# Optimization experiments

Measured on AMD Instinct MI355X. Metric: run time of the kernel, lower is better.

## Reference

```python
import jax, jax.numpy as jnp
import numpy as np

N, C, H, K, HID = 131072, 256, 8, 128, 1024
SCALE = (C // H) ** -0.5  # 1/sqrt(32)


def layernorm(x, g, b, eps=1e-5):
    mu = jnp.mean(x, axis=-1, keepdims=True)
    var = jnp.var(x, axis=-1, keepdims=True)
    return (x - mu) * jax.lax.rsqrt(var + eps) * g + b


def setup_inputs() -> dict:
    key = jax.random.key(0)
    ks = jax.random.split(key, 8)
    feat = jax.random.normal(ks[0], (N, C), dtype=jnp.float32)
    order = jax.random.permutation(ks[1], N)  # serialized order (gather)
    inverse = jnp.argsort(order)              # scatter back (unpad identity)
    s = 0.02
    return {
        "feat": feat,
        "ln1_g": jnp.ones((C,), jnp.float32), "ln1_b": jnp.zeros((C,), jnp.float32),
        "w_qkv": jax.random.normal(ks[2], (C, 3 * C), jnp.float32) * s,
        "b_qkv": jnp.zeros((3 * C,), jnp.float32),
        "w_proj": jax.random.normal(ks[3], (C, C), jnp.float32) * s,
        "b_proj": jnp.zeros((C,), jnp.float32),
        "ln2_g": jnp.ones((C,), jnp.float32), "ln2_b": jnp.zeros((C,), jnp.float32),
        "w1": jax.random.normal(ks[4], (C, HID), jnp.float32) * s,
        "b1": jnp.zeros((HID,), jnp.float32),
        "w2": jax.random.normal(ks[5], (HID, C), jnp.float32) * s,
        "b2": jnp.zeros((C,), jnp.float32),
        "order": order,
        "inverse": inverse,
    }


def attention(x, w_qkv, b_qkv, w_proj, b_proj, order, inverse):
    D = C // H
    qkv = x @ w_qkv + b_qkv                       # [N, 3C]
    qkv = qkv[order]                              # gather to serialized order
    qkv = qkv.reshape(-1, K, 3, H, D)             # [P, K, 3, H, D]
    q, k, v = jnp.moveaxis(qkv, 2, 0)             # each [P, K, H, D]
    q = jnp.swapaxes(q, 1, 2)                     # [P, H, K, D]
    k = jnp.swapaxes(k, 1, 2)
    v = jnp.swapaxes(v, 1, 2)
    attn = jnp.einsum("phkd,phjd->phkj", q * SCALE, k)  # [P, H, K, K]
    attn = jax.nn.softmax(attn, axis=-1)
    out = jnp.einsum("phkj,phjd->phkd", attn, v)  # [P, H, K, D]
    out = jnp.swapaxes(out, 1, 2).reshape(-1, C)  # [N, C]
    out = out[inverse]                            # scatter back to input order
    return out @ w_proj + b_proj


def reference(feat, ln1_g, ln1_b, w_qkv, b_qkv, w_proj, b_proj,
              ln2_g, ln2_b, w1, b1, w2, b2, order, inverse):
    # pre-norm transformer block: x + attn(ln1(x)); x + mlp(ln2(x))
    x = feat
    x = x + attention(layernorm(x, ln1_g, ln1_b), w_qkv, b_qkv, w_proj, b_proj, order, inverse)
    h = layernorm(x, ln2_g, ln2_b)
    h = jax.nn.gelu(h @ w1 + b1) @ w2 + b2
    return x + h
```

## Files before the change

### kernel.cpp

```cpp
#include <hip/hip_runtime.h>
#include <hip/hip_bf16.h>

typedef __hip_bfloat16 bf16;
typedef __bf16 bf16x8 __attribute__((ext_vector_type(8)));
typedef float f32x4 __attribute__((ext_vector_type(4)));

#define N_TOK 131072
#define C_DIM 256
#define HID_DIM 1024

__device__ __forceinline__ void async_copy16(void* lds, const void* g) {
  __builtin_amdgcn_global_load_lds(
      (const __attribute__((address_space(1))) void*)g,
      (__attribute__((address_space(3))) void*)lds, 16, 0, 0);
}

__device__ __forceinline__ float fast_rcp(float x) {
#if __has_builtin(__builtin_amdgcn_rcpf)
  return __builtin_amdgcn_rcpf(x);
#else
  return 1.f / x;
#endif
}

__device__ __forceinline__ float fast_gelu(float x) {
  float y = 0.7978845608028654f * x * (1.f + 0.044715f * x * x);
  float e = __expf(2.f * y);
  float th = 1.f - 2.f * fast_rcp(e + 1.f);
  return 0.5f * x * (1.f + th);
}

__global__ void ln_bf16_kernel(const float* __restrict__ x,
                               const float* __restrict__ g,
                               const float* __restrict__ b,
                               bf16* __restrict__ out) {
  int row = blockIdx.x * 4 + threadIdx.y;
  int lane = threadIdx.x;
  size_t base = (size_t)row * C_DIM + lane * 4;
  float4 v = *(const float4*)(x + base);
  float s = v.x + v.y + v.z + v.w;
  float s2 = v.x * v.x + v.y * v.y + v.z * v.z + v.w * v.w;
#pragma unroll
  for (int m = 1; m < 64; m <<= 1) { s += __shfl_xor(s, m); s2 += __shfl_xor(s2, m); }
  float mean = s * (1.f / 256.f);
  float var = s2 * (1.f / 256.f) - mean * mean;
  float rstd = rsqrtf(var + 1e-5f);
  float4 gv = *(const float4*)(g + lane * 4);
  float4 bv = *(const float4*)(b + lane * 4);
  union { bf16 h[4]; uint2 u; } pk;
  pk.h[0] = __float2bfloat16((v.x - mean) * rstd * gv.x + bv.x);
  pk.h[1] = __float2bfloat16((v.y - mean) * rstd * gv.y + bv.y);
  pk.h[2] = __float2bfloat16((v.z - mean) * rstd * gv.z + bv.z);
  pk.h[3] = __float2bfloat16((v.w - mean) * rstd * gv.w + bv.w);
  *(uint2*)(out + base) = pk.u;
}

__global__ void cast_transpose_kernel(const float* __restrict__ in, bf16* __restrict__ out,
                                      int K, int N) {
  int idx = blockIdx.x * 256 + threadIdx.x;
  if (idx >= K * N) return;
  int n = idx / K, k = idx - n * K;
  out[idx] = __float2bfloat16(in[(size_t)k * N + n]);
}

template <int EPI>
__global__ __launch_bounds__(256) void gemm_bt_kernel(
    const bf16* __restrict__ A, const bf16* __restrict__ Bt,
    const float* __restrict__ bias, const float* __restrict__ res,
    void* __restrict__ outp, int K, int ldn) {
  __shared__ bf16 sA[128 * 64];
  __shared__ bf16 sB[128 * 64];
  const int tid = threadIdx.x;
  const int wid = tid >> 6;
  const int lane = tid & 63;
  const int quad = lane >> 4;
  const int l16 = lane & 15;
  const int n0 = blockIdx.x * 128;
  const int m0 = blockIdx.y * 128;
  const int wm = (wid >> 1) * 64;
  const int wn = (wid & 1) * 64;
  const int srow = tid >> 3;
  const int scol = ((tid & 7) ^ (srow & 7)) * 8;

  const bf16* pA = A + (size_t)(m0 + srow) * K + scol;
  const bf16* pB = Bt + (size_t)(n0 + srow) * K + scol;
  const size_t isStride = (size_t)32 * K;

  f32x4 acc[4][4] = {};

  for (int k0 = 0; k0 < K; k0 += 64) {
#pragma unroll
    for (int is = 0; is < 4; ++is) {
      async_copy16(&sA[is * 2048 + wid * 512], pA + is * isStride);
      async_copy16(&sB[is * 2048 + wid * 512], pB + is * isStride);
    }
    pA += 64;
    pB += 64;
    __syncthreads();
#pragma unroll
    for (int kk = 0; kk < 64; kk += 32) {
      bf16x8 af[4], bfr[4];
#pragma unroll
      for (int i = 0; i < 4; ++i)
        af[i] = *(const bf16x8*)&sA[(wm + i * 16 + l16) * 64 +
                                    ((((kk >> 3) + quad) ^ (l16 & 7)) << 3)];
#pragma unroll
      for (int j = 0; j < 4; ++j)
        bfr[j] = *(const bf16x8*)&sB[(wn + j * 16 + l16) * 64 +
                                     ((((kk >> 3) + quad) ^ (l16 & 7)) << 3)];
#pragma unroll
      for (int i = 0; i < 4; ++i)
#pragma unroll
        for (int j = 0; j < 4; ++j)
          acc[i][j] = __builtin_amdgcn_mfma_f32_16x16x32_bf16(af[i], bfr[j], acc[i][j], 0, 0, 0);
    }
    __syncthreads();
  }

  float bv[4];
#pragma unroll
  for (int j = 0; j < 4; ++j) bv[j] = bias[n0 + wn + j * 16 + l16];
  const int colb = n0 + wn + l16;
#pragma unroll
  for (int i = 0; i < 4; ++i) {
    int rowb = m0 + wm + i * 16 + quad * 4;
#pragma unroll
    for (int r = 0; r < 4; ++r) {
      size_t rowoff = (size_t)(rowb + r) * ldn + colb;
#pragma unroll
      for (int j = 0; j < 4; ++j) {
        size_t idx = rowoff + j * 16;
        float v = acc[i][j][r] + bv[j];
        if constexpr (EPI == 0) {
          ((bf16*)outp)[idx] = __float2bfloat16(v);
        } else if constexpr (EPI == 1) {
          ((float*)outp)[idx] = v + res[idx];
        } else if constexpr (EPI == 2) {
          ((bf16*)outp)[idx] = __float2bfloat16(fast_gelu(v));
        } else {
          ((float*)outp)[idx] = v + res[idx];
        }
      }
    }
  }
}

__global__ __launch_bounds__(256) void attn_kernel(
    const bf16* __restrict__ qkv, const int* __restrict__ order,
    bf16* __restrict__ outw) {
  __shared__ bf16 sK[128 * 40];
  __shared__ bf16 sVt[32 * 136];
  __shared__ bf16 sP[128 * 136];
  __shared__ int sOrd[128];
  const int h = blockIdx.x;
  const int p = blockIdx.y;
  const int tid = threadIdx.x;
  const int wid = tid >> 6;
  const int lane = tid & 63;
  const int quad = lane >> 4;
  const int l16 = lane & 15;

  if (tid < 128) sOrd[tid] = order[p * 128 + tid];
  __syncthreads();

  {
    int r = tid >> 1;
    int half = (tid & 1) * 16;
    size_t base = (size_t)sOrd[r] * 768 + h * 32;
    uint4 ka = *(const uint4*)&qkv[base + 256 + half];
    uint4 kb = *(const uint4*)&qkv[base + 256 + half + 8];
    *(uint4*)&sK[r * 40 + half] = ka;
    *(uint4*)&sK[r * 40 + half + 8] = kb;
    union { uint4 u[2]; bf16 e[16]; } vv;
    vv.u[0] = *(const uint4*)&qkv[base + 512 + half];
    vv.u[1] = *(const uint4*)&qkv[base + 512 + half + 8];
#pragma unroll
    for (int c = 0; c < 16; ++c) sVt[(half + c) * 136 + r] = vv.e[c];
  }
  __syncthreads();

  bf16x8 qf[2];
#pragma unroll
  for (int t = 0; t < 2; ++t) {
    int r = wid * 32 + t * 16 + l16;
    qf[t] = *(const bf16x8*)&qkv[(size_t)sOrd[r] * 768 + h * 32 + quad * 8];
  }

  const f32x4 zero = {0.f, 0.f, 0.f, 0.f};
  f32x4 s[2][8];
#pragma unroll
  for (int ct = 0; ct < 8; ++ct) {
    bf16x8 kf = *(const bf16x8*)&sK[(ct * 16 + l16) * 40 + quad * 8];
#pragma unroll
    for (int t = 0; t < 2; ++t)
      s[t][ct] = __builtin_amdgcn_mfma_f32_16x16x32_bf16(qf[t], kf, zero, 0, 0, 0);
  }

  const float scale = 0.17677669529663687f;
#pragma unroll
  for (int t = 0; t < 2; ++t) {
#pragma unroll
    for (int r = 0; r < 4; ++r) {
      float mx = -1e30f;
#pragma unroll
      for (int ct = 0; ct < 8; ++ct) mx = fmaxf(mx, s[t][ct][r]);
      mx *= scale;
#pragma unroll
      for (int mk = 1; mk < 16; mk <<= 1) mx = fmaxf(mx, __shfl_xor(mx, mk));
      float sum = 0.f;
#pragma unroll
      for (int ct = 0; ct < 8; ++ct) {
        float e = __expf(scale * s[t][ct][r] - mx);
        s[t][ct][r] = e;
        sum += e;
      }
#pragma unroll
      for (int mk = 1; mk < 16; mk <<= 1) sum += __shfl_xor(sum, mk);
      float inv = fast_rcp(sum);
      int prow = wid * 32 + t * 16 + quad * 4 + r;
#pragma unroll
      for (int ct = 0; ct < 8; ++ct)
        sP[prow * 136 + ct * 16 + l16] = __float2bfloat16(s[t][ct][r] * inv);
    }
  }
  __syncthreads();

  f32x4 o[2][2] = {};
#pragma unroll
  for (int ks = 0; ks < 4; ++ks) {
    bf16x8 vf[2];
#pragma unroll
    for (int n = 0; n < 2; ++n)
      vf[n] = *(const bf16x8*)&sVt[(n * 16 + l16) * 136 + ks * 32 + quad * 8];
#pragma unroll
    for (int t = 0; t < 2; ++t) {
      bf16x8 pf = *(const bf16x8*)&sP[(wid * 32 + t * 16 + l16) * 136 + ks * 32 + quad * 8];
#pragma unroll
      for (int n = 0; n < 2; ++n)
        o[t][n] = __builtin_amdgcn_mfma_f32_16x16x32_bf16(pf, vf[n], o[t][n], 0, 0, 0);
    }
  }

#pragma unroll
  for (int t = 0; t < 2; ++t) {
    int rowb = wid * 32 + t * 16 + quad * 4;
#pragma unroll
    for (int r = 0; r < 4; ++r) {
      size_t gbase = (size_t)sOrd[rowb + r] * 256 + h * 32;
#pragma unroll
      for (int n = 0; n < 2; ++n)
        outw[gbase + n * 16 + l16] = __float2bfloat16(o[t][n][r]);
    }
  }
}

extern "C" void kernel_launch(void* const* d_in, const int* in_sizes, int n_in,
                              void* d_out, int out_size, void* d_ws, size_t ws_size,
                              hipStream_t stream) {
  const float* feat   = (const float*)d_in[0];
  const float* ln1_g  = (const float*)d_in[1];
  const float* ln1_b  = (const float*)d_in[2];
  const float* w_qkv  = (const float*)d_in[3];
  const float* b_qkv  = (const float*)d_in[4];
  const float* w_proj = (const float*)d_in[5];
  const float* b_proj = (const float*)d_in[6];
  const float* ln2_g  = (const float*)d_in[7];
  const float* ln2_b  = (const float*)d_in[8];
  const float* w1     = (const float*)d_in[9];
  const float* b1     = (const float*)d_in[10];
  const float* w2     = (const float*)d_in[11];
  const float* b2     = (const float*)d_in[12];
  const int* order    = (const int*)d_in[13];
  float* out = (float*)d_out;

  char* ws = (char*)d_ws;
  size_t off = 0;
  auto take = [&](size_t bytes) {
    char* pp = ws + off;
    off += (bytes + 255) & ~(size_t)255;
    return pp;
  };
  bf16* ln_buf  = (bf16*)take((size_t)N_TOK * 256 * 2);
  bf16* qkv     = (bf16*)take((size_t)N_TOK * 768 * 2);
  bf16* attn_o  = (bf16*)take((size_t)N_TOK * 256 * 2);
  float* xres   = (float*)take((size_t)N_TOK * 256 * 4);
  bf16* wqkvT   = (bf16*)take(768 * 256 * 2);
  bf16* wprojT  = (bf16*)take(256 * 256 * 2);
  bf16* w1T     = (bf16*)take(1024 * 256 * 2);
  bf16* w2T     = (bf16*)take(256 * 1024 * 2);
  bf16* hbuf    = qkv;

  cast_transpose_kernel<<<768, 256, 0, stream>>>(w_qkv, wqkvT, 256, 768);
  cast_transpose_kernel<<<256, 256, 0, stream>>>(w_proj, wprojT, 256, 256);
  cast_transpose_kernel<<<1024, 256, 0, stream>>>(w1, w1T, 256, 1024);
  cast_transpose_kernel<<<1024, 256, 0, stream>>>(w2, w2T, 1024, 256);

  ln_bf16_kernel<<<N_TOK / 4, dim3(64, 4), 0, stream>>>(feat, ln1_g, ln1_b, ln_buf);
  gemm_bt_kernel<0><<<dim3(6, 1024), 256, 0, stream>>>(ln_buf, wqkvT, b_qkv, nullptr, qkv, 256, 768);
  attn_kernel<<<dim3(8, 1024), 256, 0, stream>>>(qkv, order, attn_o);
  gemm_bt_kernel<1><<<dim3(2, 1024), 256, 0, stream>>>(attn_o, wprojT, b_proj, feat, xres, 256, 256);
  ln_bf16_kernel<<<N_TOK / 4, dim3(64, 4), 0, stream>>>(xres, ln2_g, ln2_b, ln_buf);
  gemm_bt_kernel<2><<<dim3(8, 1024), 256, 0, stream>>>(ln_buf, w1T, b1, nullptr, hbuf, 256, 1024);
  gemm_bt_kernel<3><<<dim3(2, 1024), 256, 0, stream>>>(hbuf, w2T, b2, xres, out, 1024, 256);
}
```

Before: 868.3 us.

## Remap block indices for XCD-local L2 reuse, simplify GELU and bf16 rounding

Flattens the GEMM and attention grids to 1-D and remaps block ids so that blocks sharing the same A row-tile (or the same attention partition across heads) run on the same XCD. The intent is better L2 reuse of activations on the multi-XCD MI355X. It also rewrites GELU as x*sigmoid(k*x) with fused constants, and replaces __float2bfloat16 with a manual round-to-nearest-even bit trick that skips NaN handling. Together these aim to cut memory traffic and epilogue ALU cost. The risk is that the bf16 conversion no longer treats NaN specially.

```diff
diff --git a/kernel.cpp b/kernel.cpp
--- a/kernel.cpp
+++ b/kernel.cpp
@@ -23,11 +23,19 @@
 #endif
 }
 
+__device__ __forceinline__ bf16 bf16_rne(float f) {
+  unsigned u = __float_as_uint(f);
+  u += 0x7FFF + ((u >> 16) & 1);
+  unsigned short s = (unsigned short)(u >> 16);
+  return *reinterpret_cast<bf16*>(&s);
+}
+
 __device__ __forceinline__ float fast_gelu(float x) {
-  float y = 0.7978845608028654f * x * (1.f + 0.044715f * x * x);
-  float e = __expf(2.f * y);
-  float th = 1.f - 2.f * fast_rcp(e + 1.f);
-  return 0.5f * x * (1.f + th);
+  float t = x * x;
+  float u = __builtin_fmaf(0.07135481627f, t, 1.5957691216f);
+  float z = x * u;
+  float e = __expf(-z);
+  return x * fast_rcp(1.f + e);
 }
 
 __global__ void ln_bf16_kernel(const float* __restrict__ x,
@@ -48,10 +56,10 @@
   float4 gv = *(const float4*)(g + lane * 4);
   float4 bv = *(const float4*)(b + lane * 4);
   union { bf16 h[4]; uint2 u; } pk;
-  pk.h[0] = __float2bfloat16((v.x - mean) * rstd * gv.x + bv.x);
-  pk.h[1] = __float2bfloat16((v.y - mean) * rstd * gv.y + bv.y);
-  pk.h[2] = __float2bfloat16((v.z - mean) * rstd * gv.z + bv.z);
-  pk.h[3] = __float2bfloat16((v.w - mean) * rstd * gv.w + bv.w);
+  pk.h[0] = bf16_rne((v.x - mean) * rstd * gv.x + bv.x);
+  pk.h[1] = bf16_rne((v.y - mean) * rstd * gv.y + bv.y);
+  pk.h[2] = bf16_rne((v.z - mean) * rstd * gv.z + bv.z);
+  pk.h[3] = bf16_rne((v.w - mean) * rstd * gv.w + bv.w);
   *(uint2*)(out + base) = pk.u;
 }
 
@@ -60,23 +68,26 @@
   int idx = blockIdx.x * 256 + threadIdx.x;
   if (idx >= K * N) return;
   int n = idx / K, k = idx - n * K;
-  out[idx] = __float2bfloat16(in[(size_t)k * N + n]);
-}
-
-template <int EPI>
+  out[idx] = bf16_rne(in[(size_t)k * N + n]);
+}
+
+template <int EPI, int NXT>
 __global__ __launch_bounds__(256) void gemm_bt_kernel(
     const bf16* __restrict__ A, const bf16* __restrict__ Bt,
     const float* __restrict__ bias, const float* __restrict__ res,
     void* __restrict__ outp, int K, int ldn) {
   __shared__ bf16 sA[128 * 64];
   __shared__ bf16 sB[128 * 64];
+  const int bid = blockIdx.x;
+  const int xcd = bid & 7;
+  const int j = bid >> 3;
+  const int n0 = (j % NXT) * 128;
+  const int m0 = ((j / NXT) * 8 + xcd) * 128;
   const int tid = threadIdx.x;
   const int wid = tid >> 6;
   const int lane = tid & 63;
   const int quad = lane >> 4;
   const int l16 = lane & 15;
-  const int n0 = blockIdx.x * 128;
-  const int m0 = blockIdx.y * 128;
   const int wm = (wid >> 1) * 64;
   const int wn = (wid & 1) * 64;
   const int srow = tid >> 3;
@@ -105,21 +116,21 @@
         af[i] = *(const bf16x8*)&sA[(wm + i * 16 + l16) * 64 +
                                     ((((kk >> 3) + quad) ^ (l16 & 7)) << 3)];
 #pragma unroll
-      for (int j = 0; j < 4; ++j)
-        bfr[j] = *(const bf16x8*)&sB[(wn + j * 16 + l16) * 64 +
-                                     ((((kk >> 3) + quad) ^ (l16 & 7)) << 3)];
+      for (int j2 = 0; j2 < 4; ++j2)
+        bfr[j2] = *(const bf16x8*)&sB[(wn + j2 * 16 + l16) * 64 +
+                                      ((((kk >> 3) + quad) ^ (l16 & 7)) << 3)];
 #pragma unroll
       for (int i = 0; i < 4; ++i)
 #pragma unroll
-        for (int j = 0; j < 4; ++j)
-          acc[i][j] = __builtin_amdgcn_mfma_f32_16x16x32_bf16(af[i], bfr[j], acc[i][j], 0, 0, 0);
+        for (int j2 = 0; j2 < 4; ++j2)
+          acc[i][j2] = __builtin_amdgcn_mfma_f32_16x16x32_bf16(af[i], bfr[j2], acc[i][j2], 0, 0, 0);
     }
     __syncthreads();
   }
 
   float bv[4];
 #pragma unroll
-  for (int j = 0; j < 4; ++j) bv[j] = bias[n0 + wn + j * 16 + l16];
+  for (int j2 = 0; j2 < 4; ++j2) bv[j2] = bias[n0 + wn + j2 * 16 + l16];
   const int colb = n0 + wn + l16;
 #pragma unroll
   for (int i = 0; i < 4; ++i) {
@@ -128,15 +139,15 @@
     for (int r = 0; r < 4; ++r) {
       size_t rowoff = (size_t)(rowb + r) * ldn + colb;
 #pragma unroll
-      for (int j = 0; j < 4; ++j) {
-        size_t idx = rowoff + j * 16;
-        float v = acc[i][j][r] + bv[j];
+      for (int j2 = 0; j2 < 4; ++j2) {
+        size_t idx = rowoff + j2 * 16;
+        float v = acc[i][j2][r] + bv[j2];
         if constexpr (EPI == 0) {
-          ((bf16*)outp)[idx] = __float2bfloat16(v);
+          ((bf16*)outp)[idx] = bf16_rne(v);
         } else if constexpr (EPI == 1) {
           ((float*)outp)[idx] = v + res[idx];
         } else if constexpr (EPI == 2) {
-          ((bf16*)outp)[idx] = __float2bfloat16(fast_gelu(v));
+          ((bf16*)outp)[idx] = bf16_rne(fast_gelu(v));
         } else {
           ((float*)outp)[idx] = v + res[idx];
         }
@@ -152,8 +163,9 @@
   __shared__ bf16 sVt[32 * 136];
   __shared__ bf16 sP[128 * 136];
   __shared__ int sOrd[128];
-  const int h = blockIdx.x;
-  const int p = blockIdx.y;
+  const int bid = blockIdx.x;
+  const int h = (bid >> 3) & 7;
+  const int p = ((bid >> 6) << 3) | (bid & 7);
   const int tid = threadIdx.x;
   const int wid = tid >> 6;
   const int lane = tid & 63;
@@ -220,7 +232,7 @@
       int prow = wid * 32 + t * 16 + quad * 4 + r;
 #pragma unroll
       for (int ct = 0; ct < 8; ++ct)
-        sP[prow * 136 + ct * 16 + l16] = __float2bfloat16(s[t][ct][r] * inv);
+        sP[prow * 136 + ct * 16 + l16] = bf16_rne(s[t][ct][r] * inv);
     }
   }
   __syncthreads();
@@ -249,7 +261,7 @@
       size_t gbase = (size_t)sOrd[rowb + r] * 256 + h * 32;
 #pragma unroll
       for (int n = 0; n < 2; ++n)
-        outw[gbase + n * 16 + l16] = __float2bfloat16(o[t][n][r]);
+        outw[gbase + n * 16 + l16] = bf16_rne(o[t][n][r]);
     }
   }
 }
@@ -296,10 +308,10 @@
   cast_transpose_kernel<<<1024, 256, 0, stream>>>(w2, w2T, 1024, 256);
 
   ln_bf16_kernel<<<N_TOK / 4, dim3(64, 4), 0, stream>>>(feat, ln1_g, ln1_b, ln_buf);
-  gemm_bt_kernel<0><<<dim3(6, 1024), 256, 0, stream>>>(ln_buf, wqkvT, b_qkv, nullptr, qkv, 256, 768);
-  attn_kernel<<<dim3(8, 1024), 256, 0, stream>>>(qkv, order, attn_o);
-  gemm_bt_kernel<1><<<dim3(2, 1024), 256, 0, stream>>>(attn_o, wprojT, b_proj, feat, xres, 256, 256);
+  gemm_bt_kernel<0, 6><<<6 * 1024, 256, 0, stream>>>(ln_buf, wqkvT, b_qkv, nullptr, qkv, 256, 768);
+  attn_kernel<<<8 * 1024, 256, 0, stream>>>(qkv, order, attn_o);
+  gemm_bt_kernel<1, 2><<<2 * 1024, 256, 0, stream>>>(attn_o, wprojT, b_proj, feat, xres, 256, 256);
   ln_bf16_kernel<<<N_TOK / 4, dim3(64, 4), 0, stream>>>(xres, ln2_g, ln2_b, ln_buf);
-  gemm_bt_kernel<2><<<dim3(8, 1024), 256, 0, stream>>>(ln_buf, w1T, b1, nullptr, hbuf, 256, 1024);
-  gemm_bt_kernel<3><<<dim3(2, 1024), 256, 0, stream>>>(hbuf, w2T, b2, xres, out, 1024, 256);
-}
+  gemm_bt_kernel<2, 8><<<8 * 1024, 256, 0, stream>>>(ln_buf, w1T, b1, nullptr, hbuf, 256, 1024);
+  gemm_bt_kernel<3, 2><<<2 * 1024, 256, 0, stream>>>(hbuf, w2T, b2, xres, out, 1024, 256);
+}
```

Result: faster. 832.6 us (-4.1%).
